# Kernel optimization log

Hardware: AMD Instinct MI355X
Metric: run time of the kernel (lower is better)

The kernel has to match this reference:

```python
import jax, jax.numpy as jnp
import numpy as np
from jax import lax

DIM = 128
HEADS = 4
B, H, W = 8, 128, 128


def conv1x1(x, w, b):
    # x: [B,C,H,W], w: [O,I,1,1]
    y = lax.conv_general_dilated(x, w, (1, 1), 'VALID',
                                 dimension_numbers=('NCHW', 'OIHW', 'NCHW'))
    return y + b[None, :, None, None]


def dwconv3x3(x, w, b):
    # depthwise: w: [C,1,3,3], groups=C
    C = x.shape[1]
    y = lax.conv_general_dilated(x, w, (1, 1), ((1, 1), (1, 1)),
                                 dimension_numbers=('NCHW', 'OIHW', 'NCHW'),
                                 feature_group_count=C)
    return y + b[None, :, None, None]


def setup_inputs() -> dict:
    key = jax.random.key(0)
    ks = jax.random.split(key, 7)
    s = 0.02
    return {
        'x': jax.random.normal(ks[0], (B, DIM, H, W), jnp.float32),
        'qkv_w': jax.random.normal(ks[1], (3 * DIM, DIM, 1, 1), jnp.float32) * s,
        'qkv_b': jnp.zeros((3 * DIM,), jnp.float32),
        'dw_w': jax.random.normal(ks[2], (3 * DIM, 1, 3, 3), jnp.float32) * s,
        'dw_b': jnp.zeros((3 * DIM,), jnp.float32),
        'proj_w': jax.random.normal(ks[3], (DIM, DIM, 1, 1), jnp.float32) * s,
        'proj_b': jnp.zeros((DIM,), jnp.float32),
        'temperature': jnp.ones((HEADS, 1, 1, 1), jnp.float32),
    }


def reference(x, qkv_w, qkv_b, dw_w, dw_b, proj_w, proj_b, temperature):
    b, C, h, w = x.shape
    heads = temperature.shape[0]
    c = C // heads

    qkv = dwconv3x3(conv1x1(x, qkv_w, qkv_b), dw_w, dw_b)
    q, k, v = jnp.split(qkv, 3, axis=1)

    # b (head c) h w -> b head c h w
    q = q.reshape(b, heads, c, h, w)
    k = k.reshape(b, heads, c, h, w)
    v = v.reshape(b, heads, c, h, w)

    # L2-normalize along H (axis=-2), matching torch F.normalize eps=1e-12
    eps = 1e-12
    q = q / jnp.maximum(jnp.linalg.norm(q, axis=-2, keepdims=True), eps)
    k = k / jnp.maximum(jnp.linalg.norm(k, axis=-2, keepdims=True), eps)

    # attn[b,n,c,j,k] = sum_i q[b,n,c,i,j] * k_[b,n,c,i,k]  -> [b,head,c,W,W]
    attn = jnp.einsum('bncij,bncik->bncjk', q, k) * temperature
    attn = jax.nn.softmax(attn, axis=-2)

    # out[b,n,c,i,k] = sum_j v[b,n,c,i,j] * attn[b,n,c,j,k]
    out = jnp.einsum('bncij,bncjk->bncik', v, attn)
    out = out.reshape(b, C, h, w)
    return conv1x1(out, proj_w, proj_b)
```

## Files before the change

kernel.cpp:

```cpp
#include <hip/hip_runtime.h>

typedef unsigned short u16;
typedef unsigned int   u32;

typedef short bf16x8 __attribute__((ext_vector_type(8)));
typedef float f32x4  __attribute__((ext_vector_type(4)));

__device__ __forceinline__ float bf2f(u16 u) { return __uint_as_float(((u32)u) << 16); }
__device__ __forceinline__ u16 f2bf(float f) {
    u32 u = __float_as_uint(f);
    return (u16)((u + 0x7fffu + ((u >> 16) & 1u)) >> 16);
}

#define MFMA16(a, b, c) __builtin_amdgcn_mfma_f32_16x16x32_bf16(a, b, c, 0, 0, 0)

__global__ __launch_bounds__(256, 4) void k_xpose(const float* __restrict__ x,
                                                  u16* __restrict__ xT) {
    __shared__ u16 Xs[128 * 128];
    const int ptile = blockIdx.x, b = blockIdx.y;
    const int t = threadIdx.x;
    const float* xb = x + (((size_t)b) << 21) + ptile * 128;
#pragma unroll
    for (int i = 0; i < 16; ++i) {
        int idx = i * 256 + t;
        int ci = idx >> 5, pq = idx & 31;
        float4 v = *(const float4*)(xb + (((size_t)ci) << 14) + pq * 4);
        u32 lo = (u32)f2bf(v.x) | ((u32)f2bf(v.y) << 16);
        u32 hi = (u32)f2bf(v.z) | ((u32)f2bf(v.w) << 16);
        uint2 pk; pk.x = lo; pk.y = hi;
        int cq = ci >> 3;
        *(uint2*)(&Xs[ci * 128 + ((pq ^ cq) << 2)]) = pk;
    }
    __syncthreads();
    u16* ob = xT + (((size_t)b) << 21) + ((size_t)(ptile * 128)) * 128;
#pragma unroll
    for (int j = 0; j < 8; ++j) {
        int p = j * 16 + (t >> 4), cq = t & 15;
        u16 tmp[8];
#pragma unroll
        for (int c = 0; c < 8; ++c) {
            int ci = cq * 8 + c;
            tmp[c] = Xs[ci * 128 + (((p >> 2) ^ cq) << 2) + (p & 3)];
        }
        *(uint4*)(&ob[(size_t)p * 128 + cq * 8]) = *(const uint4*)tmp;
    }
}

__global__ __launch_bounds__(512, 2) void k_qkv(const u16* __restrict__ xT,
                                                const float* __restrict__ w,
                                                const float* __restrict__ bias,
                                                u16* __restrict__ out1) {
    extern __shared__ char smem[];
    u16* Bt = (u16*)smem;
    u16* Cs = Bt + 2048 * 8;
    const int h = blockIdx.x, cg = blockIdx.y, b = blockIdx.z;
    const int t = threadIdx.x;

    const u16* xb = xT + (((size_t)b) << 21) + ((size_t)(h * 128)) * 128;
#pragma unroll
    for (int i = 0; i < 4; ++i) {
        int slot = i * 512 + t;
        int p = slot >> 4, g = slot & 15;
        int gg = g ^ (p & 15);
        uint4 v = *(const uint4*)(&xb[p * 128 + gg * 8]);
        *(uint4*)(&Bt[slot * 8]) = v;
    }

    const int wave = t >> 6, lane = t & 63, m16 = lane & 15, quad = lane >> 4;
    bf16x8 afr[4];
    {
        const float* wp0 = w + (size_t)(cg * 128 + wave * 16 + m16) * 128 + quad * 8;
#pragma unroll
        for (int kk = 0; kk < 4; ++kk) {
            float4 w0 = *(const float4*)(wp0 + kk * 32);
            float4 w1 = *(const float4*)(wp0 + kk * 32 + 4);
            bf16x8 a;
            a[0] = (short)f2bf(w0.x); a[1] = (short)f2bf(w0.y);
            a[2] = (short)f2bf(w0.z); a[3] = (short)f2bf(w0.w);
            a[4] = (short)f2bf(w1.x); a[5] = (short)f2bf(w1.y);
            a[6] = (short)f2bf(w1.z); a[7] = (short)f2bf(w1.w);
            afr[kk] = a;
        }
    }
    __syncthreads();

    f32x4 acc[8] = {};
#pragma unroll
    for (int kk = 0; kk < 4; ++kk) {
        const int g = kk * 4 + quad;
#pragma unroll
        for (int nt = 0; nt < 8; ++nt) {
            int p = nt * 16 + m16;
            bf16x8 bf = *(const bf16x8*)(&Bt[p * 128 + ((g ^ (p & 15)) << 3)]);
            acc[nt] = MFMA16(afr[kk], bf, acc[nt]);
        }
    }

    float bv[4];
#pragma unroll
    for (int r = 0; r < 4; ++r) bv[r] = bias[cg * 128 + wave * 16 + quad * 4 + r];
#pragma unroll
    for (int nt = 0; nt < 8; ++nt) {
        int p = nt * 16 + m16;
#pragma unroll
        for (int r = 0; r < 4; ++r)
            Cs[(wave * 16 + quad * 4 + r) * 136 + p] = f2bf(acc[nt][r] + bv[r]);
    }
    __syncthreads();

    u16* ob = out1 + (((size_t)(b * 384 + cg * 128)) << 14) + (h << 7);
#pragma unroll
    for (int it = 0; it < 4; ++it) {
        int idx = it * 512 + t;
        int co = idx >> 4, cp = idx & 15;
        *(uint4*)(&ob[((size_t)co << 14) + cp * 8]) = *(const uint4*)(&Cs[co * 136 + cp * 8]);
    }
}

__global__ __launch_bounds__(256, 4) void k_dw(const u16* __restrict__ in,
                                               const float* __restrict__ w,
                                               const float* __restrict__ bias,
                                               u16* __restrict__ out) {
    __shared__ u16 tile[34 * 144];
    const int htile = blockIdx.x;
    const int ch = blockIdx.y;
    const int b = blockIdx.z;
    const int t = threadIdx.x;
    const u16* base = in + (((size_t)(b * 384 + ch)) << 14);

    if (t < 68) {
        int r = t >> 1, side = t & 1;
        uint4 z = {0, 0, 0, 0};
        *(uint4*)(&tile[r * 144 + side * 136]) = z;
    }
    for (int it = 0; it < 3; ++it) {
        int idx = it * 256 + t;
        if (idx < 544) {
            int r = idx >> 4, cq = idx & 15;
            int y = htile * 32 - 1 + r;
            uint4 v = {0, 0, 0, 0};
            if (y >= 0 && y <= 127) v = *(const uint4*)(base + (y << 7) + cq * 8);
            *(uint4*)(&tile[r * 144 + 8 + cq * 8]) = v;
        }
    }
    float wg[9];
#pragma unroll
    for (int i = 0; i < 9; ++i) wg[i] = w[ch * 9 + i];
    const float bv = bias[ch];
    __syncthreads();

    const int r = t >> 4, cp = t & 15, c0 = cp * 8;
    u16* ob = out + (((size_t)(b * 384 + ch)) << 14) + ((htile * 32) << 7) + c0;
#pragma unroll
    for (int half = 0; half < 2; ++half) {
        const int ro = r + half * 16;
        float acc[8];
#pragma unroll
        for (int c = 0; c < 8; ++c) acc[c] = bv;
#pragma unroll
        for (int dy = 0; dy < 3; ++dy) {
            const u16* row = &tile[(ro + dy) * 144 + 8 + c0];
            float v[10];
            v[0] = bf2f(row[-1]);
            uint4 m = *(const uint4*)row;
            v[1] = bf2f((u16)(m.x & 0xffff)); v[2] = bf2f((u16)(m.x >> 16));
            v[3] = bf2f((u16)(m.y & 0xffff)); v[4] = bf2f((u16)(m.y >> 16));
            v[5] = bf2f((u16)(m.z & 0xffff)); v[6] = bf2f((u16)(m.z >> 16));
            v[7] = bf2f((u16)(m.w & 0xffff)); v[8] = bf2f((u16)(m.w >> 16));
            v[9] = bf2f(row[8]);
#pragma unroll
            for (int dx = 0; dx < 3; ++dx) {
                const float wv = wg[dy * 3 + dx];
#pragma unroll
                for (int c = 0; c < 8; ++c) acc[c] += wv * v[c + dx];
            }
        }
        u32 pk[4];
#pragma unroll
        for (int c2 = 0; c2 < 4; ++c2) {
            u32 lo = f2bf(acc[2 * c2]), hi = f2bf(acc[2 * c2 + 1]);
            pk[c2] = lo | (hi << 16);
        }
        *(uint4*)(ob + (ro << 7)) = *(uint4*)pk;
    }
}

__global__ __launch_bounds__(512, 1) void k_attn(const u16* __restrict__ qkv,
                                                 const float* __restrict__ temp,
                                                 u16* __restrict__ outp) {
    extern __shared__ char smem[];
    u16* Qt = (u16*)smem;
    u16* Kt = Qt + 128 * 136;
    u16* Vs = Kt + 128 * 136;
    u16* Pt = Vs + 128 * 136;
    float* rq = (float*)(Pt + 128 * 136);
    float* rk = rq + 128;
    float* St = (float*)smem;
    u16* Osh = (u16*)smem;

    const int ch = blockIdx.x, b = blockIdx.y;
    const int head = ch >> 5;
    const int t = threadIdx.x;
    const size_t qoff = ((size_t)(b * 384 + ch)) << 14;
    const size_t koff = ((size_t)(b * 384 + 128 + ch)) << 14;
    const size_t voff = ((size_t)(b * 384 + 256 + ch)) << 14;

    for (int it = 0; it < 4; ++it) {
        int idx = it * 512 + t;
        int row = idx >> 4, cp = idx & 15;
        *(uint4*)(&Vs[row * 136 + cp * 8]) = *(const uint4*)(&qkv[voff + (row << 7) + cp * 8]);
    }
    for (int it = 0; it < 32; ++it) {
        int idx = it * 512 + t;
        int i = idx >> 7, j = idx & 127;
        Qt[j * 136 + i] = qkv[qoff + (i << 7) + j];
        Kt[j * 136 + i] = qkv[koff + (i << 7) + j];
    }
    __syncthreads();

    if (t < 256) {
        const u16* rowp = (t < 128) ? &Qt[t * 136] : &Kt[(t - 128) * 136];
        float s = 0.f;
#pragma unroll
        for (int c = 0; c < 16; ++c) {
            uint4 v = *(const uint4*)(rowp + c * 8);
            float f0 = bf2f((u16)(v.x & 0xffff)), f1 = bf2f((u16)(v.x >> 16));
            float f2 = bf2f((u16)(v.y & 0xffff)), f3 = bf2f((u16)(v.y >> 16));
            float f4 = bf2f((u16)(v.z & 0xffff)), f5 = bf2f((u16)(v.z >> 16));
            float f6 = bf2f((u16)(v.w & 0xffff)), f7 = bf2f((u16)(v.w >> 16));
            s += f0 * f0 + f1 * f1 + f2 * f2 + f3 * f3 + f4 * f4 + f5 * f5 + f6 * f6 + f7 * f7;
        }
        float r = 1.0f / fmaxf(sqrtf(s), 1e-12f);
        if (t < 128) rq[t] = r; else rk[t - 128] = r;
    }
    __syncthreads();

    const int wave = t >> 6, lane = t & 63, m16 = lane & 15, quad = lane >> 4;

    f32x4 acc[8] = {};
    for (int kk = 0; kk < 4; ++kk) {
        const int kb = kk * 32 + quad * 8;
        bf16x8 a = *(const bf16x8*)(&Qt[(wave * 16 + m16) * 136 + kb]);
#pragma unroll
        for (int nt = 0; nt < 8; ++nt) {
            bf16x8 bf = *(const bf16x8*)(&Kt[(nt * 16 + m16) * 136 + kb]);
            acc[nt] = MFMA16(a, bf, acc[nt]);
        }
    }
    const float tv = temp[head];
    float rqv[4];
#pragma unroll
    for (int r = 0; r < 4; ++r) rqv[r] = rq[wave * 16 + quad * 4 + r] * tv;
    __syncthreads();
#pragma unroll
    for (int nt = 0; nt < 8; ++nt) {
        int kcol = nt * 16 + m16;
        float rkv = rk[kcol];
        f32x4 v = acc[nt], o;
        o[0] = v[0] * rqv[0] * rkv; o[1] = v[1] * rqv[1] * rkv;
        o[2] = v[2] * rqv[2] * rkv; o[3] = v[3] * rqv[3] * rkv;
        *(f32x4*)(&St[kcol * 132 + wave * 16 + quad * 4]) = o;
    }
    __syncthreads();

    {
        const int col = t >> 2, part = t & 3;
        const float* Srow = &St[col * 132 + part * 32];
        float e[32];
#pragma unroll
        for (int c = 0; c < 8; ++c) {
            f32x4 v = *(const f32x4*)(&Srow[c * 4]);
            e[c * 4 + 0] = v[0]; e[c * 4 + 1] = v[1]; e[c * 4 + 2] = v[2]; e[c * 4 + 3] = v[3];
        }
        float lmax = -1e30f;
#pragma unroll
        for (int jj = 0; jj < 32; ++jj) lmax = fmaxf(lmax, e[jj]);
        lmax = fmaxf(lmax, __shfl_xor(lmax, 1));
        lmax = fmaxf(lmax, __shfl_xor(lmax, 2));
        float lsum = 0.f;
#pragma unroll
        for (int jj = 0; jj < 32; ++jj) { e[jj] = __expf(e[jj] - lmax); lsum += e[jj]; }
        lsum += __shfl_xor(lsum, 1);
        lsum += __shfl_xor(lsum, 2);
        float inv = 1.0f / lsum;
        u32* prow = (u32*)&Pt[col * 136 + part * 32];
#pragma unroll
        for (int c2 = 0; c2 < 16; ++c2) {
            u32 lo = f2bf(e[2 * c2] * inv), hi = f2bf(e[2 * c2 + 1] * inv);
            prow[c2] = lo | (hi << 16);
        }
    }
    __syncthreads();

    f32x4 acc2[8] = {};
    for (int kk = 0; kk < 4; ++kk) {
        const int kb = kk * 32 + quad * 8;
        bf16x8 a = *(const bf16x8*)(&Vs[(wave * 16 + m16) * 136 + kb]);
#pragma unroll
        for (int nt = 0; nt < 8; ++nt) {
            bf16x8 bf = *(const bf16x8*)(&Pt[(nt * 16 + m16) * 136 + kb]);
            acc2[nt] = MFMA16(a, bf, acc2[nt]);
        }
    }
#pragma unroll
    for (int nt = 0; nt < 8; ++nt) {
        int kcol = nt * 16 + m16;
#pragma unroll
        for (int r = 0; r < 4; ++r)
            Osh[(wave * 16 + quad * 4 + r) * 136 + kcol] = f2bf(acc2[nt][r]);
    }
    __syncthreads();

    u16* ob = outp + (((size_t)(b * 128 + ch)) << 14);
    for (int it = 0; it < 4; ++it) {
        int idx = it * 512 + t;
        int row = idx >> 4, cp = idx & 15;
        *(uint4*)(&ob[(row << 7) + cp * 8]) = *(const uint4*)(&Osh[row * 136 + cp * 8]);
    }
}

__global__ __launch_bounds__(512, 1) void k_proj(const u16* __restrict__ ain,
                                                 const float* __restrict__ w,
                                                 const float* __restrict__ bias,
                                                 float* __restrict__ outp) {
    extern __shared__ char smem[];
    u16* xT = (u16*)smem;
    float* Cs = (float*)(xT + 128 * 136);
    const int h = blockIdx.x, b = blockIdx.y;
    const int t = threadIdx.x;

    const u16* ab = ain + (((size_t)(b * 128)) << 14) + (h << 7);
    for (int it = 0; it < 32; ++it) {
        int idx = it * 512 + t;
        int ci = idx >> 7, p = idx & 127;
        xT[p * 136 + ci] = ab[((size_t)ci << 14) + p];
    }
    __syncthreads();

    const int wave = t >> 6, lane = t & 63, m16 = lane & 15, quad = lane >> 4;
    f32x4 acc[8] = {};
    for (int kk = 0; kk < 4; ++kk) {
        const int kb = kk * 32 + quad * 8;
        const float* wp = w + (wave * 16 + m16) * 128 + kb;
        float4 w0 = *(const float4*)wp;
        float4 w1 = *(const float4*)(wp + 4);
        bf16x8 a;
        a[0] = (short)f2bf(w0.x); a[1] = (short)f2bf(w0.y);
        a[2] = (short)f2bf(w0.z); a[3] = (short)f2bf(w0.w);
        a[4] = (short)f2bf(w1.x); a[5] = (short)f2bf(w1.y);
        a[6] = (short)f2bf(w1.z); a[7] = (short)f2bf(w1.w);
#pragma unroll
        for (int nt = 0; nt < 8; ++nt) {
            bf16x8 bf = *(const bf16x8*)(&xT[(nt * 16 + m16) * 136 + kb]);
            acc[nt] = MFMA16(a, bf, acc[nt]);
        }
    }
    float bv[4];
#pragma unroll
    for (int r = 0; r < 4; ++r) bv[r] = bias[wave * 16 + quad * 4 + r];
#pragma unroll
    for (int nt = 0; nt < 8; ++nt) {
        int p = nt * 16 + m16;
#pragma unroll
        for (int r = 0; r < 4; ++r)
            Cs[(wave * 16 + quad * 4 + r) * 132 + p] = acc[nt][r] + bv[r];
    }
    __syncthreads();

    float* ob = outp + (((size_t)(b * 128)) << 14) + (h << 7);
    for (int it = 0; it < 8; ++it) {
        int idx = it * 512 + t;
        int row = idx >> 5, cp = idx & 31;
        *(float4*)(&ob[((size_t)row << 14) + cp * 4]) = *(const float4*)(&Cs[row * 132 + cp * 4]);
    }
}

extern "C" void kernel_launch(void* const* d_in, const int* in_sizes, int n_in,
                              void* d_out, int out_size, void* d_ws, size_t ws_size,
                              hipStream_t stream) {
    const float* x      = (const float*)d_in[0];
    const float* qkv_w  = (const float*)d_in[1];
    const float* qkv_b  = (const float*)d_in[2];
    const float* dw_w   = (const float*)d_in[3];
    const float* dw_b   = (const float*)d_in[4];
    const float* proj_w = (const float*)d_in[5];
    const float* proj_b = (const float*)d_in[6];
    const float* temp   = (const float*)d_in[7];
    float* out = (float*)d_out;

    u16* buf1 = (u16*)d_ws;
    u16* buf2 = buf1 + (size_t)8 * 384 * 16384;

    hipFuncSetAttribute((const void*)k_qkv,  hipFuncAttributeMaxDynamicSharedMemorySize, 67584);
    hipFuncSetAttribute((const void*)k_attn, hipFuncAttributeMaxDynamicSharedMemorySize, 140288);
    hipFuncSetAttribute((const void*)k_proj, hipFuncAttributeMaxDynamicSharedMemorySize, 102400);

    k_xpose<<<dim3(128, 8), 256, 0, stream>>>(x, buf2);
    k_qkv<<<dim3(128, 3, 8), 512, 67584, stream>>>(buf2, qkv_w, qkv_b, buf1);
    k_dw<<<dim3(4, 384, 8), 256, 0, stream>>>(buf1, dw_w, dw_b, buf2);
    k_attn<<<dim3(128, 8), 512, 140288, stream>>>(buf2, temp, buf1);
    k_proj<<<dim3(128, 8), 512, 102400, stream>>>(buf1, proj_w, proj_b, out);
}
```

Measured before the change: 271.0 us.

## Restructure attention kernel: swizzled LDS, register softmax, V in registers

Rewrites k_attn so that V fragments load straight from global memory into registers. Q and K are transposed through a small staging buffer into XOR-swizzled, unpadded LDS tiles, and the sum of squares is accumulated during that transpose. The softmax is computed directly on the MFMA accumulators using cross-lane shuffles, which removes the fp32 score round trip through LDS. Shared memory drops from about 137KB to 76KB so more blocks can fit per CU, at the cost of more barriers in the transpose loop and higher register pressure.

Result: faster. 258.9 us (-4.5%).

```diff
diff --git a/kernel.cpp b/kernel.cpp
--- a/kernel.cpp
+++ b/kernel.cpp
@@ -185,18 +185,18 @@
     }
 }
 
-__global__ __launch_bounds__(512, 1) void k_attn(const u16* __restrict__ qkv,
+__global__ __launch_bounds__(512, 4) void k_attn(const u16* __restrict__ qkv,
                                                  const float* __restrict__ temp,
                                                  u16* __restrict__ outp) {
     extern __shared__ char smem[];
     u16* Qt = (u16*)smem;
-    u16* Kt = Qt + 128 * 136;
-    u16* Vs = Kt + 128 * 136;
-    u16* Pt = Vs + 128 * 136;
-    float* rq = (float*)(Pt + 128 * 136);
-    float* rk = rq + 128;
-    float* St = (float*)smem;
-    u16* Osh = (u16*)smem;
+    u16* Kt = Qt + 16384;
+    u16* Sg = Qt + 32768;
+    float* ps = (float*)(smem + 74752);
+    float* rq = (float*)(smem + 76800);
+    float* rk = (float*)(smem + 77312);
+    u16* Pt = Qt;
+    u16* Osh = Kt;
 
     const int ch = blockIdx.x, b = blockIdx.y;
     const int head = ch >> 5;
@@ -205,117 +205,133 @@
     const size_t koff = ((size_t)(b * 384 + 128 + ch)) << 14;
     const size_t voff = ((size_t)(b * 384 + 256 + ch)) << 14;
 
+    const int wave = t >> 6, lane = t & 63, m16 = lane & 15, quad = lane >> 4;
+
+    bf16x8 vfr[4];
+    {
+        const u16* vrow = qkv + voff + (size_t)(wave * 16 + m16) * 128 + quad * 8;
+#pragma unroll
+        for (int kk = 0; kk < 4; ++kk)
+            vfr[kk] = *(const bf16x8*)(vrow + kk * 32);
+    }
+
+    const int ldr = t >> 4, ldj8 = t & 15;
+    const size_t ldsrc = (ldr < 16 ? qoff + (size_t)ldr * 128
+                                   : koff + (size_t)(ldr - 16) * 128) + ldj8 * 8;
+    const int gmat = t >> 8, gig = (t >> 7) & 1, gj = t & 127;
+    const u16* gcol = &Sg[(gmat * 16 + gig * 8) * 144 + gj];
+    u16* gdstbase = (gmat ? Kt : Qt) + gj * 128;
+    float ssq = 0.f;
+#pragma unroll
+    for (int p = 0; p < 8; ++p) {
+        *(uint4*)(&Sg[ldr * 144 + ldj8 * 8]) = *(const uint4*)(&qkv[ldsrc + (size_t)p * 2048]);
+        __syncthreads();
+        u16 tmp[8];
+#pragma unroll
+        for (int c = 0; c < 8; ++c) {
+            u16 v = gcol[c * 144];
+            tmp[c] = v;
+            float f = bf2f(v);
+            ssq += f * f;
+        }
+        int g = p * 2 + gig;
+        *(uint4*)(gdstbase + ((g ^ (gj & 15)) << 3)) = *(const uint4*)tmp;
+        __syncthreads();
+    }
+    ps[(gmat * 2 + gig) * 128 + gj] = ssq;
+    __syncthreads();
+    if (t < 256) {
+        int mat = t >> 7, j = t & 127;
+        float s = ps[(mat * 2) * 128 + j] + ps[(mat * 2 + 1) * 128 + j];
+        float r = 1.0f / fmaxf(sqrtf(s), 1e-12f);
+        if (mat == 0) rq[j] = r; else rk[j] = r;
+    }
+    __syncthreads();
+
+    f32x4 S[8] = {};
+#pragma unroll
+    for (int kk = 0; kk < 4; ++kk) {
+        const int sw = ((kk * 4 + quad) ^ m16) << 3;
+        bf16x8 bf = *(const bf16x8*)(&Kt[(wave * 16 + m16) * 128 + sw]);
+#pragma unroll
+        for (int jt = 0; jt < 8; ++jt) {
+            bf16x8 af = *(const bf16x8*)(&Qt[(jt * 16 + m16) * 128 + sw]);
+            S[jt] = MFMA16(af, bf, S[jt]);
+        }
+    }
+
+    const float sc = temp[head] * rk[wave * 16 + m16];
+    float vals[8][4];
+    float vmax = -1e30f;
+#pragma unroll
+    for (int jt = 0; jt < 8; ++jt)
+#pragma unroll
+        for (int r = 0; r < 4; ++r) {
+            float v = S[jt][r] * (rq[jt * 16 + quad * 4 + r] * sc);
+            vals[jt][r] = v;
+            vmax = fmaxf(vmax, v);
+        }
+    vmax = fmaxf(vmax, __shfl_xor(vmax, 16));
+    vmax = fmaxf(vmax, __shfl_xor(vmax, 32));
+    float sum = 0.f;
+#pragma unroll
+    for (int jt = 0; jt < 8; ++jt)
+#pragma unroll
+        for (int r = 0; r < 4; ++r) {
+            float e = __expf(vals[jt][r] - vmax);
+            vals[jt][r] = e;
+            sum += e;
+        }
+    sum += __shfl_xor(sum, 16);
+    sum += __shfl_xor(sum, 32);
+    const float inv = 1.0f / sum;
+
+    __syncthreads();
+
+    {
+        const int k = wave * 16 + m16;
+        u16* prow = Pt + k * 128;
+#pragma unroll
+        for (int jt = 0; jt < 8; ++jt)
+#pragma unroll
+            for (int pr = 0; pr < 2; ++pr) {
+                int j0 = jt * 16 + quad * 4 + pr * 2;
+                u32 pk = (u32)f2bf(vals[jt][pr * 2] * inv) |
+                         ((u32)f2bf(vals[jt][pr * 2 + 1] * inv) << 16);
+                *(u32*)(prow + (((j0 >> 3) ^ (k & 15)) << 3) + (j0 & 7)) = pk;
+            }
+    }
+    __syncthreads();
+
+    f32x4 O[8] = {};
+#pragma unroll
+    for (int kk = 0; kk < 4; ++kk) {
+        const int sw = ((kk * 4 + quad) ^ m16) << 3;
+#pragma unroll
+        for (int nt = 0; nt < 8; ++nt) {
+            bf16x8 bf = *(const bf16x8*)(&Pt[(nt * 16 + m16) * 128 + sw]);
+            O[nt] = MFMA16(vfr[kk], bf, O[nt]);
+        }
+    }
+
+#pragma unroll
+    for (int nt = 0; nt < 8; ++nt) {
+        int k = nt * 16 + m16;
+#pragma unroll
+        for (int r = 0; r < 4; ++r) {
+            int i = wave * 16 + quad * 4 + r;
+            Osh[i * 128 + (((k >> 3) ^ (i & 15)) << 3) + (k & 7)] = f2bf(O[nt][r]);
+        }
+    }
+    __syncthreads();
+
+    u16* ob = outp + (((size_t)(b * 128 + ch)) << 14);
+#pragma unroll
     for (int it = 0; it < 4; ++it) {
         int idx = it * 512 + t;
-        int row = idx >> 4, cp = idx & 15;
-        *(uint4*)(&Vs[row * 136 + cp * 8]) = *(const uint4*)(&qkv[voff + (row << 7) + cp * 8]);
-    }
-    for (int it = 0; it < 32; ++it) {
-        int idx = it * 512 + t;
-        int i = idx >> 7, j = idx & 127;
-        Qt[j * 136 + i] = qkv[qoff + (i << 7) + j];
-        Kt[j * 136 + i] = qkv[koff + (i << 7) + j];
-    }
-    __syncthreads();
-
-    if (t < 256) {
-        const u16* rowp = (t < 128) ? &Qt[t * 136] : &Kt[(t - 128) * 136];
-        float s = 0.f;
-#pragma unroll
-        for (int c = 0; c < 16; ++c) {
-            uint4 v = *(const uint4*)(rowp + c * 8);
-            float f0 = bf2f((u16)(v.x & 0xffff)), f1 = bf2f((u16)(v.x >> 16));
-            float f2 = bf2f((u16)(v.y & 0xffff)), f3 = bf2f((u16)(v.y >> 16));
-            float f4 = bf2f((u16)(v.z & 0xffff)), f5 = bf2f((u16)(v.z >> 16));
-            float f6 = bf2f((u16)(v.w & 0xffff)), f7 = bf2f((u16)(v.w >> 16));
-            s += f0 * f0 + f1 * f1 + f2 * f2 + f3 * f3 + f4 * f4 + f5 * f5 + f6 * f6 + f7 * f7;
-        }
-        float r = 1.0f / fmaxf(sqrtf(s), 1e-12f);
-        if (t < 128) rq[t] = r; else rk[t - 128] = r;
-    }
-    __syncthreads();
-
-    const int wave = t >> 6, lane = t & 63, m16 = lane & 15, quad = lane >> 4;
-
-    f32x4 acc[8] = {};
-    for (int kk = 0; kk < 4; ++kk) {
-        const int kb = kk * 32 + quad * 8;
-        bf16x8 a = *(const bf16x8*)(&Qt[(wave * 16 + m16) * 136 + kb]);
-#pragma unroll
-        for (int nt = 0; nt < 8; ++nt) {
-            bf16x8 bf = *(const bf16x8*)(&Kt[(nt * 16 + m16) * 136 + kb]);
-            acc[nt] = MFMA16(a, bf, acc[nt]);
-        }
-    }
-    const float tv = temp[head];
-    float rqv[4];
-#pragma unroll
-    for (int r = 0; r < 4; ++r) rqv[r] = rq[wave * 16 + quad * 4 + r] * tv;
-    __syncthreads();
-#pragma unroll
-    for (int nt = 0; nt < 8; ++nt) {
-        int kcol = nt * 16 + m16;
-        float rkv = rk[kcol];
-        f32x4 v = acc[nt], o;
-        o[0] = v[0] * rqv[0] * rkv; o[1] = v[1] * rqv[1] * rkv;
-        o[2] = v[2] * rqv[2] * rkv; o[3] = v[3] * rqv[3] * rkv;
-        *(f32x4*)(&St[kcol * 132 + wave * 16 + quad * 4]) = o;
-    }
-    __syncthreads();
-
-    {
-        const int col = t >> 2, part = t & 3;
-        const float* Srow = &St[col * 132 + part * 32];
-        float e[32];
-#pragma unroll
-        for (int c = 0; c < 8; ++c) {
-            f32x4 v = *(const f32x4*)(&Srow[c * 4]);
-            e[c * 4 + 0] = v[0]; e[c * 4 + 1] = v[1]; e[c * 4 + 2] = v[2]; e[c * 4 + 3] = v[3];
-        }
-        float lmax = -1e30f;
-#pragma unroll
-        for (int jj = 0; jj < 32; ++jj) lmax = fmaxf(lmax, e[jj]);
-        lmax = fmaxf(lmax, __shfl_xor(lmax, 1));
-        lmax = fmaxf(lmax, __shfl_xor(lmax, 2));
-        float lsum = 0.f;
-#pragma unroll
-        for (int jj = 0; jj < 32; ++jj) { e[jj] = __expf(e[jj] - lmax); lsum += e[jj]; }
-        lsum += __shfl_xor(lsum, 1);
-        lsum += __shfl_xor(lsum, 2);
-        float inv = 1.0f / lsum;
-        u32* prow = (u32*)&Pt[col * 136 + part * 32];
-#pragma unroll
-        for (int c2 = 0; c2 < 16; ++c2) {
-            u32 lo = f2bf(e[2 * c2] * inv), hi = f2bf(e[2 * c2 + 1] * inv);
-            prow[c2] = lo | (hi << 16);
-        }
-    }
-    __syncthreads();
-
-    f32x4 acc2[8] = {};
-    for (int kk = 0; kk < 4; ++kk) {
-        const int kb = kk * 32 + quad * 8;
-        bf16x8 a = *(const bf16x8*)(&Vs[(wave * 16 + m16) * 136 + kb]);
-#pragma unroll
-        for (int nt = 0; nt < 8; ++nt) {
-            bf16x8 bf = *(const bf16x8*)(&Pt[(nt * 16 + m16) * 136 + kb]);
-            acc2[nt] = MFMA16(a, bf, acc2[nt]);
-        }
-    }
-#pragma unroll
-    for (int nt = 0; nt < 8; ++nt) {
-        int kcol = nt * 16 + m16;
-#pragma unroll
-        for (int r = 0; r < 4; ++r)
-            Osh[(wave * 16 + quad * 4 + r) * 136 + kcol] = f2bf(acc2[nt][r]);
-    }
-    __syncthreads();
-
-    u16* ob = outp + (((size_t)(b * 128 + ch)) << 14);
-    for (int it = 0; it < 4; ++it) {
-        int idx = it * 512 + t;
-        int row = idx >> 4, cp = idx & 15;
-        *(uint4*)(&ob[(row << 7) + cp * 8]) = *(const uint4*)(&Osh[row * 136 + cp * 8]);
+        int row = idx >> 4, gk = idx & 15;
+        uint4 v = *(const uint4*)(&Osh[row * 128 + ((gk ^ (row & 15)) << 3)]);
+        *(uint4*)(&ob[(row << 7) + gk * 8]) = v;
     }
 }
 
@@ -392,12 +408,12 @@
     u16* buf2 = buf1 + (size_t)8 * 384 * 16384;
 
     hipFuncSetAttribute((const void*)k_qkv,  hipFuncAttributeMaxDynamicSharedMemorySize, 67584);
-    hipFuncSetAttribute((const void*)k_attn, hipFuncAttributeMaxDynamicSharedMemorySize, 140288);
+    hipFuncSetAttribute((const void*)k_attn, hipFuncAttributeMaxDynamicSharedMemorySize, 77824);
     hipFuncSetAttribute((const void*)k_proj, hipFuncAttributeMaxDynamicSharedMemorySize, 102400);
 
     k_xpose<<<dim3(128, 8), 256, 0, stream>>>(x, buf2);
     k_qkv<<<dim3(128, 3, 8), 512, 67584, stream>>>(buf2, qkv_w, qkv_b, buf1);
     k_dw<<<dim3(4, 384, 8), 256, 0, stream>>>(buf1, dw_w, dw_b, buf2);
-    k_attn<<<dim3(128, 8), 512, 140288, stream>>>(buf2, temp, buf1);
+    k_attn<<<dim3(128, 8), 512, 77824, stream>>>(buf2, temp, buf1);
     k_proj<<<dim3(128, 8), 512, 102400, stream>>>(buf1, proj_w, proj_b, out);
 }
```
